# Kernel optimization log

Measured on AMD Instinct MI355X. Metric: run time of the kernel, lower is better.

## Reference

```python
import jax, jax.numpy as jnp
import numpy as np

EMBED_DIM = 1024
HIDDEN_DIM = 4096
NUM_EXPERTS = 8
TOP_K = 2


def setup_inputs() -> dict:
    key = jax.random.key(0)
    ks = jax.random.split(key, 5)
    x = jax.random.normal(ks[0], (2, 2048, EMBED_DIM), dtype=jnp.float32)
    Wg = jax.random.normal(ks[1], (EMBED_DIM, NUM_EXPERTS), dtype=jnp.float32) * 0.02
    W1 = jax.random.normal(ks[2], (NUM_EXPERTS, EMBED_DIM, HIDDEN_DIM), dtype=jnp.float32) * 0.02
    W3 = jax.random.normal(ks[3], (NUM_EXPERTS, EMBED_DIM, HIDDEN_DIM), dtype=jnp.float32) * 0.02
    W2 = jax.random.normal(ks[4], (NUM_EXPERTS, HIDDEN_DIM, EMBED_DIM), dtype=jnp.float32) * 0.02
    return {"x": x, "Wg": Wg, "W1": W1, "W3": W3, "W2": W2}


def reference(x, Wg, W1, W3, W2):
    # Gate: linear projection to num_experts logits
    gate = jnp.einsum("bsd,de->bse", x, Wg)  # [B,S,E]
    top_vals, top_idx = jax.lax.top_k(gate, TOP_K)  # [B,S,K]
    sel_w = jax.nn.softmax(top_vals, axis=-1)  # softmax over top-k values
    # Scatter selected weights into dense [B,S,E] (zeros for unselected experts)
    dense_w = jnp.sum(
        jax.nn.one_hot(top_idx, NUM_EXPERTS, dtype=sel_w.dtype) * sel_w[..., None],
        axis=-2,
    )  # [B,S,E]
    # Per-expert SwiGLU FFN; weight=0 for tokens not routed to expert e,
    # so the weighted-sum form is mathematically identical to masked dispatch.
    out = jnp.zeros_like(x)
    for e in range(NUM_EXPERTS):
        h = jax.nn.swish(jnp.einsum("bsd,dh->bsh", x, W1[e])) * jnp.einsum(
            "bsd,dh->bsh", x, W3[e]
        )
        out = out + dense_w[..., e:e + 1] * jnp.einsum("bsh,hd->bsd", h, W2[e])
    return out
```

## Files before the change

### kernel.cpp

```cpp
#include <hip/hip_runtime.h>
#include <hip/hip_bf16.h>
#include <stdint.h>

#define D_EMBED 1024
#define D_HID   4096
#define N_TOK   4096
#define N_EXP   8
#define CAP     4096
#define NROWA   8448

typedef __attribute__((ext_vector_type(4))) float f32x4;
typedef __attribute__((ext_vector_type(8))) short bf16x8;

__device__ __forceinline__ unsigned short f2bf(float f) {
    unsigned int u = __builtin_bit_cast(unsigned int, f);
    u += 0x7fffu + ((u >> 16) & 1u);
    return (unsigned short)(u >> 16);
}

__device__ __forceinline__ void gload_lds16(const void* g, void* l) {
    __builtin_amdgcn_global_load_lds(
        (const __attribute__((address_space(1))) unsigned int*)g,
        (__attribute__((address_space(3))) unsigned int*)l,
        16, 0, 0);
}

__global__ __launch_bounds__(256) void pack_w(const float* __restrict__ W,
                                              unsigned short* __restrict__ out, int R, int C) {
    int e = blockIdx.z, kb = blockIdx.y, cb = blockIdx.x;
    const float* Wp = W + (size_t)e * R * C + (size_t)(kb * 64) * C + cb * 64;
    unsigned short* op = out + (size_t)e * R * C;
    __shared__ unsigned short lds[64][72];
    int t = threadIdx.x;
    int r = t >> 2;
    int c0 = (t & 3) << 4;
    const float* src = Wp + (size_t)r * C + c0;
#pragma unroll
    for (int i = 0; i < 2; ++i) {
        f32x4 a = *reinterpret_cast<const f32x4*>(src + i * 8);
        f32x4 b = *reinterpret_cast<const f32x4*>(src + i * 8 + 4);
        bf16x8 o;
        o[0]=(short)f2bf(a[0]); o[1]=(short)f2bf(a[1]); o[2]=(short)f2bf(a[2]); o[3]=(short)f2bf(a[3]);
        o[4]=(short)f2bf(b[0]); o[5]=(short)f2bf(b[1]); o[6]=(short)f2bf(b[2]); o[7]=(short)f2bf(b[3]);
        *reinterpret_cast<bf16x8*>(&lds[r][c0 + i * 8]) = o;
    }
    __syncthreads();
#pragma unroll
    for (int i = 0; i < 2; ++i) {
        int cell = i * 256 + t;
        int ksl = cell >> 6, col = cell & 63;
        bf16x8 o;
#pragma unroll
        for (int j = 0; j < 8; ++j) o[j] = (short)lds[ksl * 8 + j][col];
        *reinterpret_cast<bf16x8*>(op + ((size_t)(kb * 8 + ksl) * C + cb * 64 + col) * 8) = o;
    }
}

__global__ __launch_bounds__(256) void pack_w13(const float* __restrict__ W1,
                                                const float* __restrict__ W3,
                                                unsigned short* __restrict__ out) {
    int e = blockIdx.z, kb = blockIdx.y, cb = blockIdx.x;
    size_t ebase = (size_t)e * D_EMBED * D_HID;
    const float* b1 = W1 + ebase + (size_t)(kb * 64) * D_HID + cb * 32;
    const float* b3 = W3 + ebase + (size_t)(kb * 64) * D_HID + cb * 32;
    unsigned short* op = out + (size_t)e * D_EMBED * 2 * D_HID;
    __shared__ unsigned short lds[64][72];
    int t = threadIdx.x;
    int r = t >> 2, ck = t & 3;
    const float* src = (ck >= 2 ? b3 : b1) + (size_t)r * D_HID + (ck & 1) * 16;
#pragma unroll
    for (int i = 0; i < 2; ++i) {
        f32x4 a = *reinterpret_cast<const f32x4*>(src + i * 8);
        f32x4 b = *reinterpret_cast<const f32x4*>(src + i * 8 + 4);
        bf16x8 o;
        o[0]=(short)f2bf(a[0]); o[1]=(short)f2bf(a[1]); o[2]=(short)f2bf(a[2]); o[3]=(short)f2bf(a[3]);
        o[4]=(short)f2bf(b[0]); o[5]=(short)f2bf(b[1]); o[6]=(short)f2bf(b[2]); o[7]=(short)f2bf(b[3]);
        *reinterpret_cast<bf16x8*>(&lds[r][ck * 16 + i * 8]) = o;
    }
    __syncthreads();
#pragma unroll
    for (int i = 0; i < 2; ++i) {
        int cell = i * 256 + t;
        int ksl = cell >> 6, pcp = cell & 63;
        int lcol = ((pcp >> 4) & 1) * 32 + ((pcp >> 5) & 1) * 16 + (pcp & 15);
        bf16x8 o;
#pragma unroll
        for (int j = 0; j < 8; ++j) o[j] = (short)lds[ksl * 8 + j][lcol];
        *reinterpret_cast<bf16x8*>(op + ((size_t)(kb * 8 + ksl) * (2 * D_HID) + cb * 64 + pcp) * 8) = o;
    }
}

__global__ __launch_bounds__(256) void gate_kernel(const float* __restrict__ x,
                                                   const float* __restrict__ Wg,
                                                   int* __restrict__ counts,
                                                   int* __restrict__ toks,
                                                   float* __restrict__ wgts,
                                                   int* __restrict__ slots) {
    int wave = threadIdx.x >> 6;
    int lane = threadIdx.x & 63;
    int tok = blockIdx.x * 4 + wave;
    const float* xp = x + (size_t)tok * D_EMBED;
    float acc[8] = {0, 0, 0, 0, 0, 0, 0, 0};
#pragma unroll
    for (int i = 0; i < 16; ++i) {
        int d = lane + 64 * i;
        float xv = xp[d];
        f32x4 w0 = *reinterpret_cast<const f32x4*>(Wg + (size_t)d * 8);
        f32x4 w1 = *reinterpret_cast<const f32x4*>(Wg + (size_t)d * 8 + 4);
        acc[0] += xv * w0[0]; acc[1] += xv * w0[1]; acc[2] += xv * w0[2]; acc[3] += xv * w0[3];
        acc[4] += xv * w1[0]; acc[5] += xv * w1[1]; acc[6] += xv * w1[2]; acc[7] += xv * w1[3];
    }
#pragma unroll
    for (int e = 0; e < 8; ++e)
        for (int s = 32; s; s >>= 1) acc[e] += __shfl_xor(acc[e], s, 64);
    if (lane == 0) {
        int i0 = 0; float v0 = acc[0];
#pragma unroll
        for (int e = 1; e < 8; ++e) if (acc[e] > v0) { v0 = acc[e]; i0 = e; }
        int i1 = -1; float v1 = -1e30f;
#pragma unroll
        for (int e = 0; e < 8; ++e) if (e != i0 && acc[e] > v1) { v1 = acc[e]; i1 = e; }
        float ex = __expf(v1 - v0);
        float w0 = 1.0f / (1.0f + ex);
        float w1 = 1.0f - w0;
        int p0 = atomicAdd(&counts[i0], 1);
        toks[i0 * CAP + p0] = tok; wgts[i0 * CAP + p0] = w0; slots[i0 * CAP + p0] = 0;
        int p1 = atomicAdd(&counts[i1], 1);
        toks[i1 * CAP + p1] = tok; wgts[i1 * CAP + p1] = w1; slots[i1 * CAP + p1] = 1;
    }
}

__global__ void prefix_kernel(const int* __restrict__ counts, int* __restrict__ offsets) {
    if (threadIdx.x == 0) {
        int s = 0;
        for (int e = 0; e < N_EXP; ++e) { offsets[e] = s; s += counts[e]; }
    }
}

__global__ __launch_bounds__(256) void build_map_kernel(const int* __restrict__ counts,
                                                        const int* __restrict__ offsets,
                                                        const int* __restrict__ toks,
                                                        const int* __restrict__ slots,
                                                        int* __restrict__ tok2row) {
    int i = blockIdx.x * 256 + threadIdx.x;
    int e = i >> 12, pos = i & (CAP - 1);
    if (pos < counts[e])
        tok2row[toks[i] * 2 + slots[i]] = offsets[e] + pos;
}

__global__ __launch_bounds__(256) void gather_x_kernel(
    const float* __restrict__ x,
    const int* __restrict__ counts, const int* __restrict__ offsets,
    const int* __restrict__ toks,
    unsigned short* __restrict__ xg) {
    int rt = blockIdx.x;
    int e = -1, base = 0, rowbase = 0, cnt = 0;
    for (int ee = 0; ee < N_EXP; ++ee) {
        int c = counts[ee];
        int nt = (c + 63) >> 6;
        if (rt < base + nt) { e = ee; rowbase = (rt - base) << 6; cnt = c; break; }
        base += nt;
    }
    if (e < 0) return;
    int off = offsets[e];
    int kb = blockIdx.y;
    __shared__ unsigned short lds[64][72];
    int t = threadIdx.x;
    int r = t >> 2, ck = t & 3;
    int pos = rowbase + r;
    unsigned short tmp[16];
    if (pos < cnt) {
        int tok = toks[e * CAP + pos];
        const float* src = x + (size_t)tok * D_EMBED + kb * 64 + ck * 16;
#pragma unroll
        for (int i = 0; i < 4; ++i) {
            f32x4 v = *reinterpret_cast<const f32x4*>(src + i * 4);
#pragma unroll
            for (int j = 0; j < 4; ++j) tmp[i * 4 + j] = f2bf(v[j]);
        }
    } else {
#pragma unroll
        for (int i = 0; i < 16; ++i) tmp[i] = 0;
    }
#pragma unroll
    for (int i = 0; i < 16; ++i) lds[r][ck * 16 + i] = tmp[i];
    __syncthreads();
    int sl = t >> 5, rr = (t & 31) * 2;
#pragma unroll
    for (int w = 0; w < 2; ++w) {
        int rw = rr + w;
        if (rowbase + rw >= cnt) continue;
        bf16x8 o;
#pragma unroll
        for (int j = 0; j < 8; ++j) o[j] = (short)lds[rw][sl * 8 + j];
        *reinterpret_cast<bf16x8*>(xg + ((size_t)(kb * 8 + sl) * NROWA + off + rowbase + rw) * 8) = o;
    }
}

__global__ __launch_bounds__(512, 1) void gemm1_kernel(
    const unsigned short* __restrict__ xg,
    const unsigned short* __restrict__ wt13,
    const int* __restrict__ counts, const int* __restrict__ offsets,
    const float* __restrict__ wgts,
    unsigned short* __restrict__ hp) {
    int rt = blockIdx.y;
    int e = -1, base = 0, rowbase = 0, cnt = 0;
#pragma unroll 1
    for (int ee = 0; ee < N_EXP; ++ee) {
        int c = counts[ee];
        int nt = (c + 255) >> 8;
        if (rt < base + nt) { e = ee; rowbase = (rt - base) << 8; cnt = c; break; }
        base += nt;
    }
    if (e < 0) return;
    int off = offsets[e];
    int colp = blockIdx.x * 256;

    __shared__ __align__(16) char lds[2][65536];

    int t = threadIdx.x, lane = t & 63, w = t >> 6;
    int wr = w >> 2, wc = w & 3;
    int q = lane >> 4, p = lane & 15;

    const unsigned short* wB = wt13 + (size_t)e * D_EMBED * 2 * D_HID;
    const unsigned short* pA = xg + (size_t)(off + rowbase) * 8;

    f32x4 acc[8][4] = {};

    auto SA = [&](char* L, int kt) {
        size_t sl = (size_t)(kt * 8 + w);
#pragma unroll
        for (int i = 0; i < 4; ++i)
            gload_lds16(pA + (sl * NROWA + i * 64 + lane) * 8, L + (w * 4 + i) * 1024);
    };
    auto SB = [&](char* L, int kt) {
        size_t sl = (size_t)(kt * 8 + w);
#pragma unroll
        for (int i = 0; i < 4; ++i)
            gload_lds16(wB + (sl * (2 * D_HID) + colp + i * 64 + lane) * 8,
                        L + 32768 + (w * 4 + i) * 1024);
    };
    auto PHASE = [&](const char* L, int ks) {
        bf16x8 af[8], bfr[4];
#pragma unroll
        for (int m = 0; m < 8; ++m)
            af[m] = *reinterpret_cast<const bf16x8*>(L + (ks * 4 + q) * 4096 + (wr * 128 + m * 16 + p) * 16);
#pragma unroll
        for (int n = 0; n < 4; ++n)
            bfr[n] = *reinterpret_cast<const bf16x8*>(L + 32768 + (ks * 4 + q) * 4096 + (wc * 64 + n * 16 + p) * 16);
        __builtin_amdgcn_s_setprio(1);
#pragma unroll
        for (int n = 0; n < 4; ++n)
#pragma unroll
            for (int m = 0; m < 8; ++m)
                acc[m][n] = __builtin_amdgcn_mfma_f32_16x16x32_bf16(af[m], bfr[n], acc[m][n], 0, 0, 0);
        __builtin_amdgcn_s_setprio(0);
    };

    SA(&lds[0][0], 0); SB(&lds[0][0], 0);
#pragma unroll 1
    for (int kt = 0; kt < 16; ++kt) {
        asm volatile("s_waitcnt vmcnt(0)" ::: "memory");
        __builtin_amdgcn_s_barrier();
        asm volatile("" ::: "memory");
        const char* Lc = &lds[kt & 1][0];
        char* Ln = &lds[(kt & 1) ^ 1][0];
        if (kt < 15) SA(Ln, kt + 1);
        PHASE(Lc, 0);
        if (kt < 15) SB(Ln, kt + 1);
        PHASE(Lc, 1);
        asm volatile("" ::: "memory");
    }

#pragma unroll
    for (int m = 0; m < 8; ++m) {
#pragma unroll
        for (int reg = 0; reg < 4; ++reg) {
            int rl = wr * 128 + m * 16 + q * 4 + reg;
            int grow = rowbase + rl;
            if (grow >= cnt) continue;
            float wgt = wgts[e * CAP + grow];
            size_t row = (size_t)(off + grow);
#pragma unroll
            for (int np = 0; np < 2; ++np) {
                float a1 = acc[m][2 * np][reg];
                float a3 = acc[m][2 * np + 1][reg];
                float hv = (a1 / (1.0f + __expf(-a1))) * a3 * wgt;
                int rc = (blockIdx.x * 8 + wc * 2 + np) * 16 + p;
                hp[((size_t)(rc >> 3) * NROWA + row) * 8 + (rc & 7)] = f2bf(hv);
            }
        }
    }
}

__global__ __launch_bounds__(512, 1) void gemm2_kernel(
    const unsigned short* __restrict__ hp,
    const unsigned short* __restrict__ wt2,
    const int* __restrict__ counts, const int* __restrict__ offsets,
    float* __restrict__ pbuf) {
    int rt = blockIdx.y;
    int e = -1, base = 0, rowbase = 0, cnt = 0;
#pragma unroll 1
    for (int ee = 0; ee < N_EXP; ++ee) {
        int c = counts[ee];
        int nt = (c + 255) >> 8;
        if (rt < base + nt) { e = ee; rowbase = (rt - base) << 8; cnt = c; break; }
        base += nt;
    }
    if (e < 0) return;
    int off = offsets[e];
    int colb = blockIdx.x * 256;
    int s2 = blockIdx.z;

    __shared__ __align__(16) char lds[2][65536];

    int t = threadIdx.x, lane = t & 63, w = t >> 6;
    int wr = w >> 2, wc = w & 3;
    int q = lane >> 4, p = lane & 15;

    const unsigned short* wB = wt2 + (size_t)e * D_HID * D_EMBED;
    const unsigned short* pA = hp + (size_t)(off + rowbase) * 8;

    f32x4 acc[8][4] = {};

    auto SA = [&](char* L, int kt) {
        size_t sl = (size_t)(s2 * 128 + kt * 8 + w);
#pragma unroll
        for (int i = 0; i < 4; ++i)
            gload_lds16(pA + (sl * NROWA + i * 64 + lane) * 8, L + (w * 4 + i) * 1024);
    };
    auto SB = [&](char* L, int kt) {
        size_t sl = (size_t)(s2 * 128 + kt * 8 + w);
#pragma unroll
        for (int i = 0; i < 4; ++i)
            gload_lds16(wB + (sl * D_EMBED + colb + i * 64 + lane) * 8,
                        L + 32768 + (w * 4 + i) * 1024);
    };
    auto PHASE = [&](const char* L, int ks) {
        bf16x8 af[8], bfr[4];
#pragma unroll
        for (int m = 0; m < 8; ++m)
            af[m] = *reinterpret_cast<const bf16x8*>(L + (ks * 4 + q) * 4096 + (wr * 128 + m * 16 + p) * 16);
#pragma unroll
        for (int n = 0; n < 4; ++n)
            bfr[n] = *reinterpret_cast<const bf16x8*>(L + 32768 + (ks * 4 + q) * 4096 + (wc * 64 + n * 16 + p) * 16);
        __builtin_amdgcn_s_setprio(1);
#pragma unroll
        for (int n = 0; n < 4; ++n)
#pragma unroll
            for (int m = 0; m < 8; ++m)
                acc[m][n] = __builtin_amdgcn_mfma_f32_16x16x32_bf16(af[m], bfr[n], acc[m][n], 0, 0, 0);
        __builtin_amdgcn_s_setprio(0);
    };

    SA(&lds[0][0], 0); SB(&lds[0][0], 0);
#pragma unroll 1
    for (int kt = 0; kt < 16; ++kt) {
        asm volatile("s_waitcnt vmcnt(0)" ::: "memory");
        __builtin_amdgcn_s_barrier();
        asm volatile("" ::: "memory");
        const char* Lc = &lds[kt & 1][0];
        char* Ln = &lds[(kt & 1) ^ 1][0];
        if (kt < 15) SA(Ln, kt + 1);
        PHASE(Lc, 0);
        if (kt < 15) SB(Ln, kt + 1);
        PHASE(Lc, 1);
        asm volatile("" ::: "memory");
    }

    float* pb = pbuf + (size_t)s2 * 8192 * D_EMBED;
#pragma unroll
    for (int m = 0; m < 8; ++m)
#pragma unroll
        for (int reg = 0; reg < 4; ++reg) {
            int rl = wr * 128 + m * 16 + q * 4 + reg;
            int grow = rowbase + rl;
            if (grow >= cnt) continue;
            float* dst = pb + (size_t)(off + grow) * D_EMBED + colb + wc * 64;
#pragma unroll
            for (int n = 0; n < 4; ++n) dst[n * 16 + p] = acc[m][n][reg];
        }
}

__global__ __launch_bounds__(256) void combine_kernel(const float* __restrict__ pbuf,
                                                      const int* __restrict__ tok2row,
                                                      float* __restrict__ out) {
    int i = blockIdx.x * 256 + threadIdx.x;
    int tok = i >> 8, c = (i & 255) * 4;
    int r0 = tok2row[tok * 2], r1 = tok2row[tok * 2 + 1];
    const size_t SP = (size_t)8192 * D_EMBED;
    f32x4 s = {0.f, 0.f, 0.f, 0.f};
#pragma unroll
    for (int sp = 0; sp < 4; ++sp) {
        f32x4 a = *reinterpret_cast<const f32x4*>(pbuf + sp * SP + (size_t)r0 * D_EMBED + c);
        f32x4 b = *reinterpret_cast<const f32x4*>(pbuf + sp * SP + (size_t)r1 * D_EMBED + c);
        s = s + a + b;
    }
    *reinterpret_cast<f32x4*>(out + (size_t)tok * D_EMBED + c) = s;
}

extern "C" void kernel_launch(void* const* d_in, const int* in_sizes, int n_in,
                              void* d_out, int out_size, void* d_ws, size_t ws_size,
                              hipStream_t stream) {
    const float* x  = (const float*)d_in[0];
    const float* Wg = (const float*)d_in[1];
    const float* W1 = (const float*)d_in[2];
    const float* W3 = (const float*)d_in[3];
    const float* W2 = (const float*)d_in[4];
    float* out = (float*)d_out;

    char* ws = (char*)d_ws;
    size_t szW = (size_t)N_EXP * D_EMBED * D_HID;
    unsigned short* wt13 = (unsigned short*)ws; ws += szW * 2 * 2;
    unsigned short* wt2  = (unsigned short*)ws; ws += szW * 2;
    unsigned short* hp   = (unsigned short*)ws; ws += (size_t)(D_HID / 8) * NROWA * 8 * 2;
    unsigned short* xg   = (unsigned short*)ws; ws += (size_t)(D_EMBED / 8) * NROWA * 8 * 2;
    int*   toks    = (int*)ws;   ws += (size_t)N_EXP * CAP * 4;
    float* wgts    = (float*)ws; ws += (size_t)N_EXP * CAP * 4;
    int*   slots   = (int*)ws;   ws += (size_t)N_EXP * CAP * 4;
    int*   tok2row = (int*)ws;   ws += (size_t)N_TOK * 2 * 4;
    int*   counts  = (int*)ws;   ws += 8 * 4;
    int*   offsets = (int*)ws;   ws += 8 * 4;
    float* pbuf = (float*)wt13;

    hipMemsetAsync(counts, 0, 8 * sizeof(int), stream);

    pack_w13<<<dim3(128, 16, N_EXP), 256, 0, stream>>>(W1, W3, wt13);
    pack_w<<<dim3(D_EMBED / 64, D_HID / 64, N_EXP), 256, 0, stream>>>(W2, wt2, D_HID, D_EMBED);
    gate_kernel<<<N_TOK / 4, 256, 0, stream>>>(x, Wg, counts, toks, wgts, slots);
    prefix_kernel<<<1, 64, 0, stream>>>(counts, offsets);
    build_map_kernel<<<(N_EXP * CAP) / 256, 256, 0, stream>>>(counts, offsets, toks, slots, tok2row);
    gather_x_kernel<<<dim3(136, D_EMBED / 64), 256, 0, stream>>>(x, counts, offsets, toks, xg);
    gemm1_kernel<<<dim3(32, 39), 512, 0, stream>>>(xg, wt13, counts, offsets, wgts, hp);
    gemm2_kernel<<<dim3(4, 39, 4), 512, 0, stream>>>(hp, wt2, counts, offsets, pbuf);
    combine_kernel<<<(N_TOK * 256) / 256, 256, 0, stream>>>(pbuf, tok2row, out);
}
```

Baseline: 537.4 us.

## Use four-stage half-tile LDS pipeline with partial vmcnt waits in expert GEMMs

Both expert GEMM kernels now split each 64-wide K step into two 32-wide half-steps and cycle them through four 32KB LDS buffers, staying two half-steps ahead. Each wave issues its loads in two chunks interleaved with its MFMA groups and waits with vmcnt(4) instead of draining all outstanding loads. The aim is to keep global-to-LDS loads in flight across barriers and hide load latency better. The cost is twice as many barriers per K, and the MFMA block is split into two M halves per step.

```diff
diff --git a/kernel.cpp b/kernel.cpp
--- a/kernel.cpp
+++ b/kernel.cpp
@@ -216,59 +216,62 @@
     int off = offsets[e];
     int colp = blockIdx.x * 256;
 
-    __shared__ __align__(16) char lds[2][65536];
+    __shared__ __align__(16) char lds[4][32768];
 
     int t = threadIdx.x, lane = t & 63, w = t >> 6;
     int wr = w >> 2, wc = w & 3;
     int q = lane >> 4, p = lane & 15;
+    int w2 = w * 2;
 
     const unsigned short* wB = wt13 + (size_t)e * D_EMBED * 2 * D_HID;
     const unsigned short* pA = xg + (size_t)(off + rowbase) * 8;
 
     f32x4 acc[8][4] = {};
 
-    auto SA = [&](char* L, int kt) {
-        size_t sl = (size_t)(kt * 8 + w);
-#pragma unroll
-        for (int i = 0; i < 4; ++i)
-            gload_lds16(pA + (sl * NROWA + i * 64 + lane) * 8, L + (w * 4 + i) * 1024);
+    auto SC = [&](int h, int c) {
+        char* Ls = &lds[h & 3][0];
+        size_t gs = (size_t)(h * 4 + (c >> 2));
+        gload_lds16(pA + (gs * NROWA + (c & 3) * 64 + lane) * 8, Ls + c * 1024);
+        gload_lds16(wB + (gs * (2 * D_HID) + colp + (c & 3) * 64 + lane) * 8,
+                    Ls + 16384 + c * 1024);
     };
-    auto SB = [&](char* L, int kt) {
-        size_t sl = (size_t)(kt * 8 + w);
-#pragma unroll
-        for (int i = 0; i < 4; ++i)
-            gload_lds16(wB + (sl * (2 * D_HID) + colp + i * 64 + lane) * 8,
-                        L + 32768 + (w * 4 + i) * 1024);
-    };
-    auto PHASE = [&](const char* L, int ks) {
-        bf16x8 af[8], bfr[4];
-#pragma unroll
-        for (int m = 0; m < 8; ++m)
-            af[m] = *reinterpret_cast<const bf16x8*>(L + (ks * 4 + q) * 4096 + (wr * 128 + m * 16 + p) * 16);
-#pragma unroll
-        for (int n = 0; n < 4; ++n)
-            bfr[n] = *reinterpret_cast<const bf16x8*>(L + 32768 + (ks * 4 + q) * 4096 + (wc * 64 + n * 16 + p) * 16);
-        __builtin_amdgcn_s_setprio(1);
-#pragma unroll
-        for (int n = 0; n < 4; ++n)
-#pragma unroll
-            for (int m = 0; m < 8; ++m)
-                acc[m][n] = __builtin_amdgcn_mfma_f32_16x16x32_bf16(af[m], bfr[n], acc[m][n], 0, 0, 0);
-        __builtin_amdgcn_s_setprio(0);
-    };
-
-    SA(&lds[0][0], 0); SB(&lds[0][0], 0);
+
+    SC(0, w2); SC(0, w2 + 1);
+    SC(1, w2); SC(1, w2 + 1);
 #pragma unroll 1
-    for (int kt = 0; kt < 16; ++kt) {
-        asm volatile("s_waitcnt vmcnt(0)" ::: "memory");
+    for (int h = 0; h < 32; ++h) {
+        if (h < 30) asm volatile("s_waitcnt vmcnt(4)" ::: "memory");
+        else        asm volatile("s_waitcnt vmcnt(0)" ::: "memory");
         __builtin_amdgcn_s_barrier();
         asm volatile("" ::: "memory");
-        const char* Lc = &lds[kt & 1][0];
-        char* Ln = &lds[(kt & 1) ^ 1][0];
-        if (kt < 15) SA(Ln, kt + 1);
-        PHASE(Lc, 0);
-        if (kt < 15) SB(Ln, kt + 1);
-        PHASE(Lc, 1);
+        const char* L = &lds[h & 3][0];
+        if (h < 30) SC(h + 2, w2);
+        bf16x8 af0[4], bfr[4];
+#pragma unroll
+        for (int m = 0; m < 4; ++m)
+            af0[m] = *reinterpret_cast<const bf16x8*>(L + q * 4096 + (wr * 128 + m * 16 + p) * 16);
+#pragma unroll
+        for (int n = 0; n < 4; ++n)
+            bfr[n] = *reinterpret_cast<const bf16x8*>(L + 16384 + q * 4096 + (wc * 64 + n * 16 + p) * 16);
+        __builtin_amdgcn_s_setprio(1);
+#pragma unroll
+        for (int n = 0; n < 4; ++n)
+#pragma unroll
+            for (int m = 0; m < 4; ++m)
+                acc[m][n] = __builtin_amdgcn_mfma_f32_16x16x32_bf16(af0[m], bfr[n], acc[m][n], 0, 0, 0);
+        __builtin_amdgcn_s_setprio(0);
+        if (h < 30) SC(h + 2, w2 + 1);
+        bf16x8 af1[4];
+#pragma unroll
+        for (int m = 0; m < 4; ++m)
+            af1[m] = *reinterpret_cast<const bf16x8*>(L + q * 4096 + (wr * 128 + (m + 4) * 16 + p) * 16);
+        __builtin_amdgcn_s_setprio(1);
+#pragma unroll
+        for (int n = 0; n < 4; ++n)
+#pragma unroll
+            for (int m = 0; m < 4; ++m)
+                acc[m + 4][n] = __builtin_amdgcn_mfma_f32_16x16x32_bf16(af1[m], bfr[n], acc[m + 4][n], 0, 0, 0);
+        __builtin_amdgcn_s_setprio(0);
         asm volatile("" ::: "memory");
     }
 
@@ -312,59 +315,62 @@
     int colb = blockIdx.x * 256;
     int s2 = blockIdx.z;
 
-    __shared__ __align__(16) char lds[2][65536];
+    __shared__ __align__(16) char lds[4][32768];
 
     int t = threadIdx.x, lane = t & 63, w = t >> 6;
     int wr = w >> 2, wc = w & 3;
     int q = lane >> 4, p = lane & 15;
+    int w2 = w * 2;
 
     const unsigned short* wB = wt2 + (size_t)e * D_HID * D_EMBED;
     const unsigned short* pA = hp + (size_t)(off + rowbase) * 8;
 
     f32x4 acc[8][4] = {};
 
-    auto SA = [&](char* L, int kt) {
-        size_t sl = (size_t)(s2 * 128 + kt * 8 + w);
-#pragma unroll
-        for (int i = 0; i < 4; ++i)
-            gload_lds16(pA + (sl * NROWA + i * 64 + lane) * 8, L + (w * 4 + i) * 1024);
+    auto SC = [&](int h, int c) {
+        char* Ls = &lds[h & 3][0];
+        size_t gs = (size_t)(s2 * 128 + h * 4 + (c >> 2));
+        gload_lds16(pA + (gs * NROWA + (c & 3) * 64 + lane) * 8, Ls + c * 1024);
+        gload_lds16(wB + (gs * D_EMBED + colb + (c & 3) * 64 + lane) * 8,
+                    Ls + 16384 + c * 1024);
     };
-    auto SB = [&](char* L, int kt) {
-        size_t sl = (size_t)(s2 * 128 + kt * 8 + w);
-#pragma unroll
-        for (int i = 0; i < 4; ++i)
-            gload_lds16(wB + (sl * D_EMBED + colb + i * 64 + lane) * 8,
-                        L + 32768 + (w * 4 + i) * 1024);
-    };
-    auto PHASE = [&](const char* L, int ks) {
-        bf16x8 af[8], bfr[4];
-#pragma unroll
-        for (int m = 0; m < 8; ++m)
-            af[m] = *reinterpret_cast<const bf16x8*>(L + (ks * 4 + q) * 4096 + (wr * 128 + m * 16 + p) * 16);
-#pragma unroll
-        for (int n = 0; n < 4; ++n)
-            bfr[n] = *reinterpret_cast<const bf16x8*>(L + 32768 + (ks * 4 + q) * 4096 + (wc * 64 + n * 16 + p) * 16);
-        __builtin_amdgcn_s_setprio(1);
-#pragma unroll
-        for (int n = 0; n < 4; ++n)
-#pragma unroll
-            for (int m = 0; m < 8; ++m)
-                acc[m][n] = __builtin_amdgcn_mfma_f32_16x16x32_bf16(af[m], bfr[n], acc[m][n], 0, 0, 0);
-        __builtin_amdgcn_s_setprio(0);
-    };
-
-    SA(&lds[0][0], 0); SB(&lds[0][0], 0);
+
+    SC(0, w2); SC(0, w2 + 1);
+    SC(1, w2); SC(1, w2 + 1);
 #pragma unroll 1
-    for (int kt = 0; kt < 16; ++kt) {
-        asm volatile("s_waitcnt vmcnt(0)" ::: "memory");
+    for (int h = 0; h < 32; ++h) {
+        if (h < 30) asm volatile("s_waitcnt vmcnt(4)" ::: "memory");
+        else        asm volatile("s_waitcnt vmcnt(0)" ::: "memory");
         __builtin_amdgcn_s_barrier();
         asm volatile("" ::: "memory");
-        const char* Lc = &lds[kt & 1][0];
-        char* Ln = &lds[(kt & 1) ^ 1][0];
-        if (kt < 15) SA(Ln, kt + 1);
-        PHASE(Lc, 0);
-        if (kt < 15) SB(Ln, kt + 1);
-        PHASE(Lc, 1);
+        const char* L = &lds[h & 3][0];
+        if (h < 30) SC(h + 2, w2);
+        bf16x8 af0[4], bfr[4];
+#pragma unroll
+        for (int m = 0; m < 4; ++m)
+            af0[m] = *reinterpret_cast<const bf16x8*>(L + q * 4096 + (wr * 128 + m * 16 + p) * 16);
+#pragma unroll
+        for (int n = 0; n < 4; ++n)
+            bfr[n] = *reinterpret_cast<const bf16x8*>(L + 16384 + q * 4096 + (wc * 64 + n * 16 + p) * 16);
+        __builtin_amdgcn_s_setprio(1);
+#pragma unroll
+        for (int n = 0; n < 4; ++n)
+#pragma unroll
+            for (int m = 0; m < 4; ++m)
+                acc[m][n] = __builtin_amdgcn_mfma_f32_16x16x32_bf16(af0[m], bfr[n], acc[m][n], 0, 0, 0);
+        __builtin_amdgcn_s_setprio(0);
+        if (h < 30) SC(h + 2, w2 + 1);
+        bf16x8 af1[4];
+#pragma unroll
+        for (int m = 0; m < 4; ++m)
+            af1[m] = *reinterpret_cast<const bf16x8*>(L + q * 4096 + (wr * 128 + (m + 4) * 16 + p) * 16);
+        __builtin_amdgcn_s_setprio(1);
+#pragma unroll
+        for (int n = 0; n < 4; ++n)
+#pragma unroll
+            for (int m = 0; m < 4; ++m)
+                acc[m + 4][n] = __builtin_amdgcn_mfma_f32_16x16x32_bf16(af1[m], bfr[n], acc[m + 4][n], 0, 0, 0);
+        __builtin_amdgcn_s_setprio(0);
         asm volatile("" ::: "memory");
     }
 
```

Result: slower. 550.3 us (+2.4%).
